# Kernel optimization log

Measured on AMD Instinct MI355X. Metric: run time of the kernel, lower is better.

Reference implementation:

```python
import jax, jax.numpy as jnp
import numpy as np

N = 50000
GAMMA = 0.1

def spmm(row, col, val, x):
    # sparse [N,N] @ dense [N,D] via gather + segment-sum over destination rows
    return jax.ops.segment_sum(val[:, None] * x[col], row, num_segments=N)

def setup_inputs() -> dict:
    key = jax.random.key(0)
    ks = jax.random.split(key, 16)
    E, EK, F, H, C = 800000, 1000000, 512, 128, 40
    return {
        "fea": jax.random.normal(ks[0], (N, F), jnp.float32),
        "adj_row": jax.random.randint(ks[1], (E,), 0, N),
        "adj_col": jax.random.randint(ks[2], (E,), 0, N),
        "adj_val": jax.random.uniform(ks[3], (E,), jnp.float32),
        "knn_row": jax.random.randint(ks[4], (EK,), 0, N),
        "knn_col": jax.random.randint(ks[5], (EK,), 0, N),
        "knn_val": jax.random.uniform(ks[6], (EK,), jnp.float32),
        "W1": jax.random.normal(ks[7], (F, H), jnp.float32) * (1.0 / np.sqrt(F)),
        "b1": jnp.zeros((H,), jnp.float32),
        "W2": jax.random.normal(ks[8], (H, C), jnp.float32) * (1.0 / np.sqrt(H)),
        "b2": jnp.zeros((C,), jnp.float32),
        "score1": jax.random.normal(ks[9], (F, 1), jnp.float32),
        "score2": jax.random.normal(ks[10], (H, 1), jnp.float32),
        "sbias1": jnp.zeros((1,), jnp.float32),
        "sbias2": jnp.zeros((1,), jnp.float32),
        "Dk1": jax.random.normal(ks[11], (F, 1), jnp.float32),
        "Dk2": jax.random.normal(ks[12], (H, 1), jnp.float32),
        "Dbias1": jnp.zeros((1,), jnp.float32),
        "Dbias2": jnp.zeros((1,), jnp.float32),
    }

def simpgcn_layer(x, W, b, s_w, s_b, d_w, d_b, adj_row, adj_col, adj_val, knn_row, knn_col, knn_val):
    support = x @ W                     # [N, Dout] shared across the 3 adjacencies
    h_adj = spmm(adj_row, adj_col, adj_val, support) + b
    h_knn = spmm(knn_row, knn_col, knn_val, support) + b
    h_id = support + b                  # identity adjacency: spmm(I, support)
    s = jax.nn.sigmoid(x @ s_w + s_b)   # [N,1] learned self-loop gate
    Dk = x @ d_w + d_b                  # [N,1]
    return s * h_adj + (1.0 - s) * h_knn + GAMMA * Dk * h_id

def reference(fea, adj_row, adj_col, adj_val, knn_row, knn_col, knn_val,
              W1, b1, W2, b2, score1, score2, sbias1, sbias2,
              Dk1, Dk2, Dbias1, Dbias2):
    x = simpgcn_layer(fea, W1, b1, score1, sbias1, Dk1, Dbias1,
                      adj_row, adj_col, adj_val, knn_row, knn_col, knn_val)
    embedding = x  # dropout is identity in eval mode
    x = simpgcn_layer(x, W2, b2, score2, sbias2, Dk2, Dbias2,
                      adj_row, adj_col, adj_val, knn_row, knn_col, knn_val)
    return jax.nn.log_softmax(x, axis=1), embedding
```

## Files before the change

kernel.cpp:

```cpp
#include <hip/hip_runtime.h>
#include <hip/hip_bf16.h>
#include <cstdint>

#define GAMMA 0.1f
#define CAP 64
#define OVF_CAP 8192

typedef unsigned int  uint32;
typedef unsigned short ushort16;
typedef float f32x4 __attribute__((ext_vector_type(4)));
typedef __bf16 bf16x8 __attribute__((ext_vector_type(8)));

union U16x8 { uint4 u4; bf16x8 bv; };

static __device__ __forceinline__ ushort16 f2bf(float f) {
    union { float f; uint32 u; } x; x.f = f;
    uint32 r = (x.u + 0x7FFFu + ((x.u >> 16) & 1u)) >> 16;
    return (ushort16)r;
}
static __device__ __forceinline__ uint32 pack2bf(float lo, float hi) {
    return (uint32)f2bf(lo) | ((uint32)f2bf(hi) << 16);
}
static __device__ __forceinline__ float bflo(uint32 u) { return __uint_as_float(u << 16); }
static __device__ __forceinline__ float bfhi(uint32 u) { return __uint_as_float(u & 0xFFFF0000u); }

__global__ __launch_bounds__(256) void prep_wt(const float* __restrict__ W1,
                                               const float* __restrict__ W2,
                                               ushort16* __restrict__ W1bt,
                                               ushort16* __restrict__ W2bt) {
    int t = blockIdx.x * 256 + threadIdx.x;
    if (t < 128 * 512) { int c = t >> 9, k = t & 511; W1bt[t] = f2bf(W1[k * 128 + c]); }
    if (t < 48 * 128)  { int c = t >> 7, k = t & 127; W2bt[t] = f2bf(c < 40 ? W2[k * 40 + c] : 0.f); }
}

__global__ __launch_bounds__(256) void gemm1_scatter(
    const float* __restrict__ A, const ushort16* __restrict__ Bt,
    const float* __restrict__ s1w, const float* __restrict__ d1w,
    const float* __restrict__ s1b, const float* __restrict__ d1b,
    ushort16* __restrict__ Cb, float* __restrict__ s_out, float* __restrict__ dk_out,
    int M, int mgrid,
    const int* __restrict__ arow_, const int* __restrict__ acol_, const float* __restrict__ aval_, int E,
    const int* __restrict__ krow_, const int* __restrict__ kcol_, const float* __restrict__ kval_, int EK,
    int* __restrict__ cnt, int N,
    uint32* __restrict__ packed_a, uint32* __restrict__ packed_k,
    uint2* __restrict__ ovf_a, uint2* __restrict__ ovf_k) {
    int bid = blockIdx.x;
    if (bid >= mgrid) {
        int i = (bid - mgrid) * 256 + threadIdx.x;
        if (i < E) {
            int r = arow_[i];
            uint32 rec = ((uint32)acol_[i] << 16) | (uint32)f2bf(aval_[i]);
            int p = atomicAdd(&cnt[r], 1);
            if (p < CAP) packed_a[(size_t)r * CAP + p] = rec;
            else { int q = atomicAdd(&cnt[2 * N], 1); if (q < OVF_CAP) ovf_a[q] = make_uint2((uint32)r, rec); }
        }
        if (i < EK) {
            int r = krow_[i];
            uint32 rec = ((uint32)kcol_[i] << 16) | (uint32)f2bf(kval_[i]);
            int p = atomicAdd(&cnt[N + r], 1);
            if (p < CAP) packed_k[(size_t)r * CAP + p] = rec;
            else { int q = atomicAdd(&cnt[2 * N + 1], 1); if (q < OVF_CAP) ovf_k[q] = make_uint2((uint32)r, rec); }
        }
        return;
    }
    int w = threadIdx.x >> 6, lane = threadIdx.x & 63;
    int row16 = lane & 15, kc = lane >> 4;
    int wrow0 = bid * 64 + w * 16;
    int r = wrow0 + row16;
    int rc = min(r, M - 1);
    const float* arow = A + (size_t)rc * 512;

    f32x4 acc[8];
    #pragma unroll
    for (int c = 0; c < 8; ++c) acc[c] = (f32x4){0.f, 0.f, 0.f, 0.f};
    float sdot = 0.f, ddot = 0.f;

    for (int ks = 0; ks < 16; ++ks) {
        int kb = ks * 32 + kc * 8;
        float4 a0 = *reinterpret_cast<const float4*>(arow + kb);
        float4 a1 = *reinterpret_cast<const float4*>(arow + kb + 4);
        float4 sw0 = *reinterpret_cast<const float4*>(s1w + kb);
        float4 sw1 = *reinterpret_cast<const float4*>(s1w + kb + 4);
        float4 dw0 = *reinterpret_cast<const float4*>(d1w + kb);
        float4 dw1 = *reinterpret_cast<const float4*>(d1w + kb + 4);
        sdot += a0.x * sw0.x + a0.y * sw0.y + a0.z * sw0.z + a0.w * sw0.w +
                a1.x * sw1.x + a1.y * sw1.y + a1.z * sw1.z + a1.w * sw1.w;
        ddot += a0.x * dw0.x + a0.y * dw0.y + a0.z * dw0.z + a0.w * dw0.w +
                a1.x * dw1.x + a1.y * dw1.y + a1.z * dw1.z + a1.w * dw1.w;
        U16x8 ua;
        ua.u4 = make_uint4(pack2bf(a0.x, a0.y), pack2bf(a0.z, a0.w),
                           pack2bf(a1.x, a1.y), pack2bf(a1.z, a1.w));
        #pragma unroll
        for (int c = 0; c < 8; ++c) {
            U16x8 ub;
            ub.u4 = *reinterpret_cast<const uint4*>(Bt + (size_t)(c * 16 + row16) * 512 + kb);
            acc[c] = __builtin_amdgcn_mfma_f32_16x16x32_bf16(ua.bv, ub.bv, acc[c], 0, 0, 0);
        }
    }

    sdot += __shfl_xor(sdot, 16); sdot += __shfl_xor(sdot, 32);
    ddot += __shfl_xor(ddot, 16); ddot += __shfl_xor(ddot, 32);
    if (kc == 0 && r < M) {
        s_out[r] = 1.f / (1.f + __expf(-(sdot + s1b[0])));
        dk_out[r] = ddot + d1b[0];
    }

    #pragma unroll
    for (int c = 0; c < 8; ++c) {
        #pragma unroll
        for (int i = 0; i < 4; ++i) {
            int orow = wrow0 + (lane >> 4) * 4 + i;
            if (orow < M) Cb[(size_t)orow * 128 + c * 16 + row16] = f2bf(acc[c][i]);
        }
    }
}

__global__ __launch_bounds__(256) void gemm2_mfma(const ushort16* __restrict__ Ab,
                                                  const ushort16* __restrict__ Bt,
                                                  float* __restrict__ C,
                                                  ushort16* __restrict__ Cb,
                                                  int M) {
    int w = threadIdx.x >> 6, lane = threadIdx.x & 63;
    int row16 = lane & 15, kc = lane >> 4;
    int wrow0 = blockIdx.x * 64 + w * 16;
    int r = wrow0 + row16;
    int rc = min(r, M - 1);

    f32x4 acc[3];
    #pragma unroll
    for (int c = 0; c < 3; ++c) acc[c] = (f32x4){0.f, 0.f, 0.f, 0.f};

    #pragma unroll
    for (int ks = 0; ks < 4; ++ks) {
        int kb = ks * 32 + kc * 8;
        U16x8 ua;
        ua.u4 = *reinterpret_cast<const uint4*>(Ab + (size_t)rc * 128 + kb);
        #pragma unroll
        for (int c = 0; c < 3; ++c) {
            U16x8 ub;
            ub.u4 = *reinterpret_cast<const uint4*>(Bt + (size_t)(c * 16 + row16) * 128 + kb);
            acc[c] = __builtin_amdgcn_mfma_f32_16x16x32_bf16(ua.bv, ub.bv, acc[c], 0, 0, 0);
        }
    }

    #pragma unroll
    for (int c = 0; c < 3; ++c) {
        int col = c * 16 + row16;
        #pragma unroll
        for (int i = 0; i < 4; ++i) {
            int orow = wrow0 + (lane >> 4) * 4 + i;
            if (orow < M && col < 40) {
                C[(size_t)orow * 40 + col] = acc[c][i];
                Cb[(size_t)orow * 40 + col] = f2bf(acc[c][i]);
            }
        }
    }
}

__global__ __launch_bounds__(256) void spmm_combine1(
    const int* __restrict__ cnt,
    const uint32* __restrict__ packed_a, const uint32* __restrict__ packed_k,
    const uint2* __restrict__ ovf_a, const uint2* __restrict__ ovf_k,
    const ushort16* __restrict__ supb, const float* __restrict__ s, const float* __restrict__ dk,
    const float* __restrict__ b1,
    const float* __restrict__ s2w, const float* __restrict__ d2w,
    const float* __restrict__ s2b, const float* __restrict__ d2b,
    float* __restrict__ emb, ushort16* __restrict__ embb,
    float* __restrict__ s_out, float* __restrict__ dk_out, int N) {
    int w = threadIdx.x >> 6, lane = threadIdx.x & 63;
    int r = blockIdx.x * 4 + w;
    if (r >= N) return;
    const uint32* su = (const uint32*)supb;

    float a0 = 0.f, a1 = 0.f, k0 = 0.f, k1 = 0.f;
    {
        const uint32* pa = packed_a + (size_t)r * CAP;
        int d = min(cnt[r], CAP);
        int e = 0;
        for (; e + 2 <= d; e += 2) {
            uint32 r0 = pa[e], r1 = pa[e + 1];
            float v0 = bflo(r0), v1 = bflo(r1);
            uint32 u0 = su[((size_t)(r0 >> 16) << 6) + lane];
            uint32 u1 = su[((size_t)(r1 >> 16) << 6) + lane];
            a0 += v0 * bflo(u0) + v1 * bflo(u1);
            a1 += v0 * bfhi(u0) + v1 * bfhi(u1);
        }
        if (e < d) {
            uint32 r0 = pa[e];
            float v0 = bflo(r0);
            uint32 u0 = su[((size_t)(r0 >> 16) << 6) + lane];
            a0 += v0 * bflo(u0); a1 += v0 * bfhi(u0);
        }
    }
    {
        const uint32* pk = packed_k + (size_t)r * CAP;
        int d = min(cnt[N + r], CAP);
        int e = 0;
        for (; e + 2 <= d; e += 2) {
            uint32 r0 = pk[e], r1 = pk[e + 1];
            float v0 = bflo(r0), v1 = bflo(r1);
            uint32 u0 = su[((size_t)(r0 >> 16) << 6) + lane];
            uint32 u1 = su[((size_t)(r1 >> 16) << 6) + lane];
            k0 += v0 * bflo(u0) + v1 * bflo(u1);
            k1 += v0 * bfhi(u0) + v1 * bfhi(u1);
        }
        if (e < d) {
            uint32 r0 = pk[e];
            float v0 = bflo(r0);
            uint32 u0 = su[((size_t)(r0 >> 16) << 6) + lane];
            k0 += v0 * bflo(u0); k1 += v0 * bfhi(u0);
        }
    }
    int nova = min(cnt[2 * N], OVF_CAP);
    for (int i = 0; i < nova; ++i) {
        uint2 t = ovf_a[i];
        if ((int)t.x == r) {
            float v = bflo(t.y);
            uint32 u = su[((size_t)(t.y >> 16) << 6) + lane];
            a0 += v * bflo(u); a1 += v * bfhi(u);
        }
    }
    int novk = min(cnt[2 * N + 1], OVF_CAP);
    for (int i = 0; i < novk; ++i) {
        uint2 t = ovf_k[i];
        if ((int)t.x == r) {
            float v = bflo(t.y);
            uint32 u = su[((size_t)(t.y >> 16) << 6) + lane];
            k0 += v * bflo(u); k1 += v * bfhi(u);
        }
    }

    float si = s[r];
    float g = GAMMA * dk[r];
    uint32 ui = su[((size_t)r << 6) + lane];
    int c0i = lane * 2, c1i = lane * 2 + 1;
    float o0 = si * a0 + (1.f - si) * k0 + g * bflo(ui) + b1[c0i] * (1.f + g);
    float o1 = si * a1 + (1.f - si) * k1 + g * bfhi(ui) + b1[c1i] * (1.f + g);

    *reinterpret_cast<float2*>(emb + (size_t)r * 128 + c0i) = make_float2(o0, o1);
    ((uint32*)embb)[((size_t)r << 6) + lane] = pack2bf(o0, o1);

    float as = o0 * s2w[c0i] + o1 * s2w[c1i];
    float ad = o0 * d2w[c0i] + o1 * d2w[c1i];
    #pragma unroll
    for (int off = 32; off; off >>= 1) {
        as += __shfl_xor(as, off);
        ad += __shfl_xor(ad, off);
    }
    if (lane == 0) {
        s_out[r] = 1.f / (1.f + __expf(-(as + s2b[0])));
        dk_out[r] = ad + d2b[0];
    }
}

__global__ __launch_bounds__(256) void spmm_combine2_lsm(
    const int* __restrict__ cnt,
    const uint32* __restrict__ packed_a, const uint32* __restrict__ packed_k,
    const uint2* __restrict__ ovf_a, const uint2* __restrict__ ovf_k,
    const ushort16* __restrict__ supb, const float* __restrict__ supf,
    const float* __restrict__ s, const float* __restrict__ dk,
    const float* __restrict__ b2, float* __restrict__ out, int N) {
    int w = threadIdx.x >> 6, lane = threadIdx.x & 63;
    int r = blockIdx.x * 4 + w;
    if (r >= N) return;
    int g = lane >> 5, li = lane & 31;
    bool act = li < 20;
    const uint32* su = (const uint32*)supb;

    float a0 = 0.f, a1 = 0.f, k0 = 0.f, k1 = 0.f;
    {
        const uint32* pa = packed_a + (size_t)r * CAP;
        int d = min(cnt[r], CAP);
        for (int e = g; e < d; e += 2) {
            uint32 rec = pa[e];
            float v = bflo(rec);
            if (act) {
                uint32 u = su[(size_t)(rec >> 16) * 20 + li];
                a0 += v * bflo(u); a1 += v * bfhi(u);
            }
        }
    }
    {
        const uint32* pk = packed_k + (size_t)r * CAP;
        int d = min(cnt[N + r], CAP);
        for (int e = g; e < d; e += 2) {
            uint32 rec = pk[e];
            float v = bflo(rec);
            if (act) {
                uint32 u = su[(size_t)(rec >> 16) * 20 + li];
                k0 += v * bflo(u); k1 += v * bfhi(u);
            }
        }
    }
    int nova = min(cnt[2 * N], OVF_CAP);
    for (int i = 0; i < nova; ++i) {
        uint2 t = ovf_a[i];
        if ((int)t.x == r && g == 0 && act) {
            float v = bflo(t.y);
            uint32 u = su[(size_t)(t.y >> 16) * 20 + li];
            a0 += v * bflo(u); a1 += v * bfhi(u);
        }
    }
    int novk = min(cnt[2 * N + 1], OVF_CAP);
    for (int i = 0; i < novk; ++i) {
        uint2 t = ovf_k[i];
        if ((int)t.x == r && g == 0 && act) {
            float v = bflo(t.y);
            uint32 u = su[(size_t)(t.y >> 16) * 20 + li];
            k0 += v * bflo(u); k1 += v * bfhi(u);
        }
    }
    a0 += __shfl_xor(a0, 32); a1 += __shfl_xor(a1, 32);
    k0 += __shfl_xor(k0, 32); k1 += __shfl_xor(k1, 32);

    float si = s[r];
    float gg = GAMMA * dk[r];
    float z0 = -INFINITY, z1 = -INFINITY;
    bool lead = act && (lane < 32);
    if (lead) {
        float2 iv = *reinterpret_cast<const float2*>(supf + (size_t)r * 40 + li * 2);
        z0 = si * a0 + (1.f - si) * k0 + gg * iv.x + b2[li * 2] * (1.f + gg);
        z1 = si * a1 + (1.f - si) * k1 + gg * iv.y + b2[li * 2 + 1] * (1.f + gg);
    }
    float m = fmaxf(z0, z1);
    #pragma unroll
    for (int off = 16; off; off >>= 1) m = fmaxf(m, __shfl_xor(m, off));
    float ex = lead ? (__expf(z0 - m) + __expf(z1 - m)) : 0.f;
    #pragma unroll
    for (int off = 16; off; off >>= 1) ex += __shfl_xor(ex, off);
    float lse = m + __logf(ex);
    if (lead)
        *reinterpret_cast<float2*>(out + (size_t)r * 40 + li * 2) = make_float2(z0 - lse, z1 - lse);
}

static inline size_t align256(size_t x) { return (x + 255) & ~(size_t)255; }

extern "C" void kernel_launch(void* const* d_in, const int* in_sizes, int n_in,
                              void* d_out, int out_size, void* d_ws, size_t ws_size,
                              hipStream_t stream) {
    const int N = 50000, C = 40;

    const float* fea     = (const float*)d_in[0];
    const int*   adj_row = (const int*)d_in[1];
    const int*   adj_col = (const int*)d_in[2];
    const float* adj_val = (const float*)d_in[3];
    const int*   knn_row = (const int*)d_in[4];
    const int*   knn_col = (const int*)d_in[5];
    const float* knn_val = (const float*)d_in[6];
    const float* W1      = (const float*)d_in[7];
    const float* b1      = (const float*)d_in[8];
    const float* W2      = (const float*)d_in[9];
    const float* b2      = (const float*)d_in[10];
    const float* score1  = (const float*)d_in[11];
    const float* score2  = (const float*)d_in[12];
    const float* sbias1  = (const float*)d_in[13];
    const float* sbias2  = (const float*)d_in[14];
    const float* Dk1     = (const float*)d_in[15];
    const float* Dk2     = (const float*)d_in[16];
    const float* Dbias1  = (const float*)d_in[17];
    const float* Dbias2  = (const float*)d_in[18];

    const int E  = in_sizes[1];
    const int EK = in_sizes[4];

    float* out_lsm = (float*)d_out;
    float* emb     = out_lsm + (size_t)N * C;

    char* wp = (char*)d_ws;
    ushort16* W1bt = (ushort16*)wp; wp += align256((size_t)128 * 512 * 2);
    ushort16* W2bt = (ushort16*)wp; wp += align256((size_t)48 * 128 * 2);
    char* sup1_region = wp;          wp += align256((size_t)N * 128 * 2);
    ushort16* sup1b = (ushort16*)sup1_region;
    float* sup2     = (float*)sup1_region;
    ushort16* sup2b = (ushort16*)(sup1_region + (size_t)N * 40 * 4);
    ushort16* embb  = (ushort16*)wp; wp += align256((size_t)N * 128 * 2);
    float* s_buf  = (float*)wp; wp += align256((size_t)N * 4);
    float* dk_buf = (float*)wp; wp += align256((size_t)N * 4);
    int* cnt  = (int*)wp; wp += align256((size_t)(2 * N + 2) * 4);
    uint32* packed_a = (uint32*)wp; wp += align256((size_t)N * CAP * 4);
    uint32* packed_k = (uint32*)wp; wp += align256((size_t)N * CAP * 4);
    uint2* ovf_a = (uint2*)wp; wp += align256((size_t)OVF_CAP * 8);
    uint2* ovf_k = (uint2*)wp; wp += align256((size_t)OVF_CAP * 8);

    int egrid = (max(E, EK) + 255) / 256;
    int mgrid = (N + 63) / 64;

    prep_wt<<<256, 256, 0, stream>>>(W1, W2, W1bt, W2bt);
    hipMemsetAsync(cnt, 0, (size_t)(2 * N + 2) * 4, stream);

    gemm1_scatter<<<mgrid + egrid, 256, 0, stream>>>(
        fea, W1bt, score1, Dk1, sbias1, Dbias1, sup1b, s_buf, dk_buf, N, mgrid,
        adj_row, adj_col, adj_val, E, knn_row, knn_col, knn_val, EK,
        cnt, N, packed_a, packed_k, ovf_a, ovf_k);

    spmm_combine1<<<(N + 3) / 4, 256, 0, stream>>>(cnt, packed_a, packed_k, ovf_a, ovf_k,
                                                   sup1b, s_buf, dk_buf, b1,
                                                   score2, Dk2, sbias2, Dbias2,
                                                   emb, embb, s_buf, dk_buf, N);

    gemm2_mfma<<<mgrid, 256, 0, stream>>>(embb, W2bt, sup2, sup2b, N);

    spmm_combine2_lsm<<<(N + 3) / 4, 256, 0, stream>>>(cnt, packed_a, packed_k, ovf_a, ovf_k,
                                                       sup2b, sup2, s_buf, dk_buf,
                                                       b2, out_lsm, N);

    (void)n_in; (void)out_size; (void)ws_size;
}
```

Before: 538.0 us.

## Batch gathers in SpMM kernels, fold counter reset into prep, use 3-way lane split

Several changes at once. The zeroing of the counters moves into the prep_wt kernel, which removes a separate memset launch. The bucketed edge records are written with nontemporal stores. The spmm_combine1 gather loop now issues 8 independent row loads per iteration to raise memory-level parallelism. spmm_combine2 splits the 64 lanes into three groups of 20 that each handle different edges, then combines them with shuffles, which uses more of the wave. OVF_CAP is doubled and the overflow record packing changes. The cost is padded wasted loads on the short tail of each row.

```diff
diff --git a/kernel.cpp b/kernel.cpp
--- a/kernel.cpp
+++ b/kernel.cpp
@@ -4,7 +4,7 @@
 
 #define GAMMA 0.1f
 #define CAP 64
-#define OVF_CAP 8192
+#define OVF_CAP 16384
 
 typedef unsigned int  uint32;
 typedef unsigned short ushort16;
@@ -27,10 +27,12 @@
 __global__ __launch_bounds__(256) void prep_wt(const float* __restrict__ W1,
                                                const float* __restrict__ W2,
                                                ushort16* __restrict__ W1bt,
-                                               ushort16* __restrict__ W2bt) {
+                                               ushort16* __restrict__ W2bt,
+                                               int* __restrict__ cnt, int NC) {
     int t = blockIdx.x * 256 + threadIdx.x;
     if (t < 128 * 512) { int c = t >> 9, k = t & 511; W1bt[t] = f2bf(W1[k * 128 + c]); }
     if (t < 48 * 128)  { int c = t >> 7, k = t & 127; W2bt[t] = f2bf(c < 40 ? W2[k * 40 + c] : 0.f); }
+    for (int j = t; j < NC; j += 256 * 256) cnt[j] = 0;
 }
 
 __global__ __launch_bounds__(256) void gemm1_scatter(
@@ -49,17 +51,19 @@
         int i = (bid - mgrid) * 256 + threadIdx.x;
         if (i < E) {
             int r = arow_[i];
-            uint32 rec = ((uint32)acol_[i] << 16) | (uint32)f2bf(aval_[i]);
+            uint32 vb = (uint32)f2bf(aval_[i]);
+            uint32 rec = ((uint32)acol_[i] << 16) | vb;
             int p = atomicAdd(&cnt[r], 1);
-            if (p < CAP) packed_a[(size_t)r * CAP + p] = rec;
-            else { int q = atomicAdd(&cnt[2 * N], 1); if (q < OVF_CAP) ovf_a[q] = make_uint2((uint32)r, rec); }
+            if (p < CAP) __builtin_nontemporal_store(rec, &packed_a[(size_t)r * CAP + p]);
+            else { int q = atomicAdd(&cnt[2 * N], 1); if (q < OVF_CAP) ovf_a[q] = make_uint2((uint32)r, (uint32)acol_[i] | (vb << 16)); }
         }
         if (i < EK) {
             int r = krow_[i];
-            uint32 rec = ((uint32)kcol_[i] << 16) | (uint32)f2bf(kval_[i]);
+            uint32 vb = (uint32)f2bf(kval_[i]);
+            uint32 rec = ((uint32)kcol_[i] << 16) | vb;
             int p = atomicAdd(&cnt[N + r], 1);
-            if (p < CAP) packed_k[(size_t)r * CAP + p] = rec;
-            else { int q = atomicAdd(&cnt[2 * N + 1], 1); if (q < OVF_CAP) ovf_k[q] = make_uint2((uint32)r, rec); }
+            if (p < CAP) __builtin_nontemporal_store(rec, &packed_k[(size_t)r * CAP + p]);
+            else { int q = atomicAdd(&cnt[2 * N + 1], 1); if (q < OVF_CAP) ovf_k[q] = make_uint2((uint32)r, (uint32)kcol_[i] | (vb << 16)); }
         }
         return;
     }
@@ -167,7 +171,7 @@
     const float* __restrict__ s2b, const float* __restrict__ d2b,
     float* __restrict__ emb, ushort16* __restrict__ embb,
     float* __restrict__ s_out, float* __restrict__ dk_out, int N) {
-    int w = threadIdx.x >> 6, lane = threadIdx.x & 63;
+    int w = threadIdx.x >> 6, l = threadIdx.x & 63;
     int r = blockIdx.x * 4 + w;
     if (r >= N) return;
     const uint32* su = (const uint32*)supb;
@@ -176,69 +180,61 @@
     {
         const uint32* pa = packed_a + (size_t)r * CAP;
         int d = min(cnt[r], CAP);
-        int e = 0;
-        for (; e + 2 <= d; e += 2) {
-            uint32 r0 = pa[e], r1 = pa[e + 1];
-            float v0 = bflo(r0), v1 = bflo(r1);
-            uint32 u0 = su[((size_t)(r0 >> 16) << 6) + lane];
-            uint32 u1 = su[((size_t)(r1 >> 16) << 6) + lane];
-            a0 += v0 * bflo(u0) + v1 * bflo(u1);
-            a1 += v0 * bfhi(u0) + v1 * bfhi(u1);
-        }
-        if (e < d) {
-            uint32 r0 = pa[e];
-            float v0 = bflo(r0);
-            uint32 u0 = su[((size_t)(r0 >> 16) << 6) + lane];
-            a0 += v0 * bflo(u0); a1 += v0 * bfhi(u0);
+        for (int e = 0; e < d; e += 8) {
+            uint32 rec[8], uu[8];
+            #pragma unroll
+            for (int j = 0; j < 8; ++j) rec[j] = pa[min(e + j, d - 1)];
+            #pragma unroll
+            for (int j = 0; j < 8; ++j) uu[j] = su[((size_t)(rec[j] >> 16) << 6) + l];
+            #pragma unroll
+            for (int j = 0; j < 8; ++j) {
+                float v = (e + j < d) ? bflo(rec[j]) : 0.f;
+                a0 += v * bflo(uu[j]); a1 += v * bfhi(uu[j]);
+            }
         }
     }
     {
         const uint32* pk = packed_k + (size_t)r * CAP;
         int d = min(cnt[N + r], CAP);
-        int e = 0;
-        for (; e + 2 <= d; e += 2) {
-            uint32 r0 = pk[e], r1 = pk[e + 1];
-            float v0 = bflo(r0), v1 = bflo(r1);
-            uint32 u0 = su[((size_t)(r0 >> 16) << 6) + lane];
-            uint32 u1 = su[((size_t)(r1 >> 16) << 6) + lane];
-            k0 += v0 * bflo(u0) + v1 * bflo(u1);
-            k1 += v0 * bfhi(u0) + v1 * bfhi(u1);
-        }
-        if (e < d) {
-            uint32 r0 = pk[e];
-            float v0 = bflo(r0);
-            uint32 u0 = su[((size_t)(r0 >> 16) << 6) + lane];
-            k0 += v0 * bflo(u0); k1 += v0 * bfhi(u0);
+        for (int e = 0; e < d; e += 8) {
+            uint32 rec[8], uu[8];
+            #pragma unroll
+            for (int j = 0; j < 8; ++j) rec[j] = pk[min(e + j, d - 1)];
+            #pragma unroll
+            for (int j = 0; j < 8; ++j) uu[j] = su[((size_t)(rec[j] >> 16) << 6) + l];
+            #pragma unroll
+            for (int j = 0; j < 8; ++j) {
+                float v = (e + j < d) ? bflo(rec[j]) : 0.f;
+                k0 += v * bflo(uu[j]); k1 += v * bfhi(uu[j]);
+            }
         }
     }
     int nova = min(cnt[2 * N], OVF_CAP);
     for (int i = 0; i < nova; ++i) {
         uint2 t = ovf_a[i];
-        if ((int)t.x == r) {
-            float v = bflo(t.y);
-            uint32 u = su[((size_t)(t.y >> 16) << 6) + lane];
-            a0 += v * bflo(u); a1 += v * bfhi(u);
-        }
+        if ((int)t.x != r) continue;
+        float v = bfhi(t.y);
+        uint32 u = su[((size_t)(t.y & 0xFFFFu) << 6) + l];
+        a0 += v * bflo(u); a1 += v * bfhi(u);
     }
     int novk = min(cnt[2 * N + 1], OVF_CAP);
     for (int i = 0; i < novk; ++i) {
         uint2 t = ovf_k[i];
-        if ((int)t.x == r) {
-            float v = bflo(t.y);
-            uint32 u = su[((size_t)(t.y >> 16) << 6) + lane];
-            k0 += v * bflo(u); k1 += v * bfhi(u);
-        }
+        if ((int)t.x != r) continue;
+        float v = bfhi(t.y);
+        uint32 u = su[((size_t)(t.y & 0xFFFFu) << 6) + l];
+        k0 += v * bflo(u); k1 += v * bfhi(u);
     }
 
     float si = s[r];
     float g = GAMMA * dk[r];
-    uint32 ui = su[((size_t)r << 6) + lane];
-    int c0i = lane * 2, c1i = lane * 2 + 1;
+    uint32 ui = su[((size_t)r << 6) + l];
+    int c0i = l * 2, c1i = l * 2 + 1;
     float o0 = si * a0 + (1.f - si) * k0 + g * bflo(ui) + b1[c0i] * (1.f + g);
     float o1 = si * a1 + (1.f - si) * k1 + g * bfhi(ui) + b1[c1i] * (1.f + g);
 
     *reinterpret_cast<float2*>(emb + (size_t)r * 128 + c0i) = make_float2(o0, o1);
-    ((uint32*)embb)[((size_t)r << 6) + lane] = pack2bf(o0, o1);
+    ((uint32*)embb)[((size_t)r << 6) + l] = pack2bf(o0, o1);
 
     float as = o0 * s2w[c0i] + o1 * s2w[c1i];
     float ad = o0 * d2w[c0i] + o1 * d2w[c1i];
@@ -247,7 +243,7 @@
         as += __shfl_xor(as, off);
         ad += __shfl_xor(ad, off);
     }
-    if (lane == 0) {
+    if (l == 0) {
         s_out[r] = 1.f / (1.f + __expf(-(as + s2b[0])));
         dk_out[r] = ad + d2b[0];
     }
@@ -260,77 +256,94 @@
     const ushort16* __restrict__ supb, const float* __restrict__ supf,
     const float* __restrict__ s, const float* __restrict__ dk,
     const float* __restrict__ b2, float* __restrict__ out, int N) {
-    int w = threadIdx.x >> 6, lane = threadIdx.x & 63;
+    int w = threadIdx.x >> 6, l = threadIdx.x & 63;
     int r = blockIdx.x * 4 + w;
     if (r >= N) return;
-    int g = lane >> 5, li = lane & 31;
-    bool act = li < 20;
+    int g = (l >= 40) ? 2 : ((l >= 20) ? 1 : 0);
+    int li = l - g * 20;
+    bool act = l < 60;
     const uint32* su = (const uint32*)supb;
 
     float a0 = 0.f, a1 = 0.f, k0 = 0.f, k1 = 0.f;
     {
         const uint32* pa = packed_a + (size_t)r * CAP;
         int d = min(cnt[r], CAP);
-        for (int e = g; e < d; e += 2) {
-            uint32 rec = pa[e];
-            float v = bflo(rec);
-            if (act) {
-                uint32 u = su[(size_t)(rec >> 16) * 20 + li];
-                a0 += v * bflo(u); a1 += v * bfhi(u);
-            }
+        for (int e = 0; e < d; e += 6) {
+            uint32 rr[6];
+            #pragma unroll
+            for (int j = 0; j < 6; ++j) rr[j] = pa[min(e + j, d - 1)];
+            uint32 rca = (g == 0) ? rr[0] : ((g == 1) ? rr[1] : rr[2]);
+            uint32 rcb = (g == 0) ? rr[3] : ((g == 1) ? rr[4] : rr[5]);
+            uint32 ua = su[(size_t)(rca >> 16) * 20 + li];
+            uint32 ub = su[(size_t)(rcb >> 16) * 20 + li];
+            float va = (act && (e + g) < d) ? bflo(rca) : 0.f;
+            float vb = (act && (e + 3 + g) < d) ? bflo(rcb) : 0.f;
+            a0 += va * bflo(ua) + vb * bflo(ub);
+            a1 += va * bfhi(ua) + vb * bfhi(ub);
         }
     }
     {
         const uint32* pk = packed_k + (size_t)r * CAP;
         int d = min(cnt[N + r], CAP);
-        for (int e = g; e < d; e += 2) {
-            uint32 rec = pk[e];
-            float v = bflo(rec);
-            if (act) {
-                uint32 u = su[(size_t)(rec >> 16) * 20 + li];
-                k0 += v * bflo(u); k1 += v * bfhi(u);
-            }
-        }
+        for (int e = 0; e < d; e += 6) {
+            uint32 rr[6];
+            #pragma unroll
+            for (int j = 0; j < 6; ++j) rr[j] = pk[min(e + j, d - 1)];
+            uint32 rca = (g == 0) ? rr[0] : ((g == 1) ? rr[1] : rr[2]);
+            uint32 rcb = (g == 0) ? rr[3] : ((g == 1) ? rr[4] : rr[5]);
+            uint32 ua = su[(size_t)(rca >> 16) * 20 + li];
+            uint32 ub = su[(size_t)(rcb >> 16) * 20 + li];
+            float va = (act && (e + g) < d) ? bflo(rca) : 0.f;
+            float vb = (act && (e + 3 + g) < d) ? bflo(rcb) : 0.f;
+            k0 += va * bflo(ua) + vb * bflo(ub);
+            k1 += va * bfhi(ua) + vb * bfhi(ub);
+        }
+    }
+    {
+        float t1, t2;
+        t1 = __shfl(a0, (l + 20) & 63); t2 = __shfl(a0, (l + 40) & 63); a0 += t1 + t2;
+        t1 = __shfl(a1, (l + 20) & 63); t2 = __shfl(a1, (l + 40) & 63); a1 += t1 + t2;
+        t1 = __shfl(k0, (l + 20) & 63); t2 = __shfl(k0, (l + 40) & 63); k0 += t1 + t2;
+        t1 = __shfl(k1, (l + 20) & 63); t2 = __shfl(k1, (l + 40) & 63); k1 += t1 + t2;
     }
     int nova = min(cnt[2 * N], OVF_CAP);
     for (int i = 0; i < nova; ++i) {
         uint2 t = ovf_a[i];
-        if ((int)t.x == r && g == 0 && act) {
-            float v = bflo(t.y);
-            uint32 u = su[(size_t)(t.y >> 16) * 20 + li];
+        if ((int)t.x != r) continue;
+        if (l < 20) {
+            float v = bfhi(t.y);
+            uint32 u = su[(size_t)(t.y & 0xFFFFu) * 20 + l];
             a0 += v * bflo(u); a1 += v * bfhi(u);
         }
     }
     int novk = min(cnt[2 * N + 1], OVF_CAP);
     for (int i = 0; i < novk; ++i) {
         uint2 t = ovf_k[i];
-        if ((int)t.x == r && g == 0 && act) {
-            float v = bflo(t.y);
-            uint32 u = su[(size_t)(t.y >> 16) * 20 + li];
+        if ((int)t.x != r) continue;
+        if (l < 20) {
+            float v = bfhi(t.y);
+            uint32 u = su[(size_t)(t.y & 0xFFFFu) * 20 + l];
             k0 += v * bflo(u); k1 += v * bfhi(u);
         }
     }
-    a0 += __shfl_xor(a0, 32); a1 += __shfl_xor(a1, 32);
-    k0 += __shfl_xor(k0, 32); k1 += __shfl_xor(k1, 32);
 
     float si = s[r];
     float gg = GAMMA * dk[r];
     float z0 = -INFINITY, z1 = -INFINITY;
-    bool lead = act && (lane < 32);
-    if (lead) {
-        float2 iv = *reinterpret_cast<const float2*>(supf + (size_t)r * 40 + li * 2);
-        z0 = si * a0 + (1.f - si) * k0 + gg * iv.x + b2[li * 2] * (1.f + gg);
-        z1 = si * a1 + (1.f - si) * k1 + gg * iv.y + b2[li * 2 + 1] * (1.f + gg);
+    if (l < 20) {
+        float2 iv = *reinterpret_cast<const float2*>(supf + (size_t)r * 40 + l * 2);
+        z0 = si * a0 + (1.f - si) * k0 + gg * iv.x + b2[l * 2] * (1.f + gg);
+        z1 = si * a1 + (1.f - si) * k1 + gg * iv.y + b2[l * 2 + 1] * (1.f + gg);
     }
     float m = fmaxf(z0, z1);
     #pragma unroll
     for (int off = 16; off; off >>= 1) m = fmaxf(m, __shfl_xor(m, off));
-    float ex = lead ? (__expf(z0 - m) + __expf(z1 - m)) : 0.f;
+    float ex = (l < 20) ? (__expf(z0 - m) + __expf(z1 - m)) : 0.f;
     #pragma unroll
     for (int off = 16; off; off >>= 1) ex += __shfl_xor(ex, off);
     float lse = m + __logf(ex);
-    if (lead)
-        *reinterpret_cast<float2*>(out + (size_t)r * 40 + li * 2) = make_float2(z0 - lse, z1 - lse);
+    if (l < 20)
+        *reinterpret_cast<float2*>(out + (size_t)r * 40 + l * 2) = make_float2(z0 - lse, z1 - lse);
 }
 
 static inline size_t align256(size_t x) { return (x + 255) & ~(size_t)255; }
@@ -385,8 +398,7 @@
     int egrid = (max(E, EK) + 255) / 256;
     int mgrid = (N + 63) / 64;
 
-    prep_wt<<<256, 256, 0, stream>>>(W1, W2, W1bt, W2bt);
-    hipMemsetAsync(cnt, 0, (size_t)(2 * N + 2) * 4, stream);
+    prep_wt<<<256, 256, 0, stream>>>(W1, W2, W1bt, W2bt, cnt, 2 * N + 2);
 
     gemm1_scatter<<<mgrid + egrid, 256, 0, stream>>>(
         fea, W1bt, score1, Dk1, sbias1, Dbias1, sup1b, s_buf, dk_buf, N, mgrid,
```

After: 488.0 us. 9.3% less time.
